# Kernel tuning notes

Measured on AMD Instinct MI355X. Metric: run time of the kernel, lower is better.

The kernel has to match this reference:

```python
import jax, jax.numpy as jnp
import numpy as np

EOS = 1e-10
ALPHA = 0.5
TEMPERATURE = 1.0
BIAS = 0.0001
N_NODES = 8192
N_EDGES = 262144
INPUT_DIM = 512
HIDDEN = 128


def setup_inputs() -> dict:
    key = jax.random.key(0)
    ks = jax.random.split(key, 7)
    features = jax.random.normal(ks[0], (N_NODES, INPUT_DIM), dtype=jnp.float32)
    W_emb = jax.random.normal(ks[1], (HIDDEN, INPUT_DIM), dtype=jnp.float32) * (1.0 / np.sqrt(INPUT_DIM))
    b_emb = jax.random.normal(ks[2], (HIDDEN,), dtype=jnp.float32) * 0.01
    W_edge = jax.random.normal(ks[3], (1, 2 * HIDDEN), dtype=jnp.float32) * (1.0 / np.sqrt(2 * HIDDEN))
    b_edge = jax.random.normal(ks[4], (1,), dtype=jnp.float32) * 0.01
    noise = jax.random.uniform(ks[5], (N_EDGES,), dtype=jnp.float32)
    edges = jax.random.randint(ks[6], (2, N_EDGES), 0, N_NODES, dtype=jnp.int64 if jax.config.jax_enable_x64 else jnp.int32)
    return {"features": features, "W_emb": W_emb, "b_emb": b_emb,
            "W_edge": W_edge, "b_edge": b_edge, "noise": noise, "edges": edges}


def _sym_normalize(adj):
    # inv_sqrt_degree[:,None] * adj * inv_sqrt_degree[None,:]
    inv_sqrt_deg = 1.0 / (jnp.sqrt(adj.sum(axis=1)) + EOS)
    return adj * inv_sqrt_deg[:, None] * inv_sqrt_deg[None, :]


def reference(features, W_emb, b_emb, W_edge, b_edge, noise, edges):
    n = N_NODES
    # node embedding: single Linear + ReLU
    h = jax.nn.relu(features @ W_emb.T + b_emb)            # [N, H]
    e0, e1 = edges[0], edges[1]
    h0, h1 = h[e0], h[e1]                                   # [E, H] gathers
    Wa, Wb = W_edge[0, :HIDDEN], W_edge[0, HIDDEN:]
    s1 = h0 @ Wa + h1 @ Wb + b_edge[0]                       # edge_mlp(cat(h0,h1))
    s2 = h1 @ Wa + h0 @ Wb + b_edge[0]                       # edge_mlp(cat(h1,h0))
    raw = 0.5 * (s1 + s2)                                    # [E]
    # gumbel gate: eps = (bias-(1-bias))*rand + (1-bias)
    eps = (BIAS - (1.0 - BIAS)) * noise + (1.0 - BIAS)
    gate = (jnp.log(eps) - jnp.log1p(-eps) + raw) / TEMPERATURE
    weights_lp = jax.nn.sigmoid(gate)                        # [E]
    weights_hp = 1.0 - weights_lp
    eye = jnp.eye(n, dtype=features.dtype)
    # scatter edge weights to dense adjacency (assignment semantics, like torch adj[e0,e1]=w)
    adj_lp = jnp.zeros((n, n), dtype=features.dtype).at[e0, e1].set(weights_lp) + eye
    adj_lp = _sym_normalize(adj_lp)
    adj_hp = jnp.zeros((n, n), dtype=features.dtype).at[e0, e1].set(weights_hp) + eye
    adj_hp = _sym_normalize(adj_hp)
    mask = jnp.zeros((n, n), dtype=features.dtype).at[e0, e1].set(1.0)
    adj_hp = eye - adj_hp * mask * ALPHA
    return (adj_lp, adj_hp, weights_lp, weights_hp)
```

## Files before the change

### kernel.cpp

```cpp
#include <hip/hip_runtime.h>
#include <cstdint>
#include <cstddef>

#define N_NODES 8192
#define N_EDGES 262144
#define INPUT_DIM 512
#define HIDDEN 128
#define ALPHA 0.5f
#define EOS 1e-10f
#define BCAP 128

typedef float v4 __attribute__((ext_vector_type(4)));
typedef __attribute__((ext_vector_type(8))) short short8;
typedef __attribute__((ext_vector_type(4))) float floatx4;

__device__ inline unsigned short f2bf(float x) {
    unsigned u = __builtin_bit_cast(unsigned, x);
    return (unsigned short)((u + 0x7FFFu + ((u >> 16) & 1u)) >> 16);
}

__global__ __launch_bounds__(256) void k0_conv(
    const float* __restrict__ F, const float* __restrict__ W,
    unsigned short* __restrict__ F16, unsigned short* __restrict__ W16,
    int* __restrict__ cnt)
{
    int t = blockIdx.x * 256 + threadIdx.x;
    if (t < N_NODES) cnt[t] = 0;
    {
        float4 v = *(const float4*)&F[(size_t)t * 4];
        uint2 p;
        p.x = (unsigned)f2bf(v.x) | ((unsigned)f2bf(v.y) << 16);
        p.y = (unsigned)f2bf(v.z) | ((unsigned)f2bf(v.w) << 16);
        *(uint2*)&F16[(size_t)t * 4] = p;
    }
    if (t < 16384) {
        float4 v = *(const float4*)&W[(size_t)t * 4];
        uint2 p;
        p.x = (unsigned)f2bf(v.x) | ((unsigned)f2bf(v.y) << 16);
        p.y = (unsigned)f2bf(v.z) | ((unsigned)f2bf(v.w) << 16);
        *(uint2*)&W16[(size_t)t * 4] = p;
    }
}

__global__ __launch_bounds__(256) void k1_g(
    const unsigned short* __restrict__ F16, const unsigned short* __restrict__ W16,
    const float* __restrict__ bemb, const float* __restrict__ Wedge,
    float* __restrict__ g)
{
    __shared__ float part[4][16];
    int tid = threadIdx.x;
    int lane = tid & 63, wave = tid >> 6;
    int ml = lane & 15, q = lane >> 4;
    int node0 = blockIdx.x * 16;
    int h0 = wave * 32;

    const unsigned short* Ap  = &F16[(size_t)(node0 + ml) * INPUT_DIM + q * 8];
    const unsigned short* Bp0 = &W16[(size_t)(h0 + ml) * INPUT_DIM + q * 8];
    const unsigned short* Bp1 = &W16[(size_t)(h0 + 16 + ml) * INPUT_DIM + q * 8];

    floatx4 acc0 = 0.f, acc1 = 0.f;
#pragma unroll 4
    for (int s = 0; s < 16; s++) {
        short8 a  = *(const short8*)(Ap  + s * 32);
        short8 b0 = *(const short8*)(Bp0 + s * 32);
        short8 b1 = *(const short8*)(Bp1 + s * 32);
        acc0 = __builtin_amdgcn_mfma_f32_16x16x32_bf16(a, b0, acc0, 0, 0, 0);
        acc1 = __builtin_amdgcn_mfma_f32_16x16x32_bf16(a, b1, acc1, 0, 0, 0);
    }
    float sr[4] = {0.f, 0.f, 0.f, 0.f};
#pragma unroll
    for (int t = 0; t < 2; t++) {
        int h = h0 + t * 16 + ml;
        float uu = Wedge[h] + Wedge[HIDDEN + h];
        float bb = bemb[h];
        floatx4 ac = t ? acc1 : acc0;
#pragma unroll
        for (int rg = 0; rg < 4; rg++) {
            float hv = ac[rg] + bb;
            sr[rg] += (hv > 0.f ? hv : 0.f) * uu;
        }
    }
#pragma unroll
    for (int m = 1; m < 16; m <<= 1) {
#pragma unroll
        for (int rg = 0; rg < 4; rg++) sr[rg] += __shfl_xor(sr[rg], m, 64);
    }
    if (ml == 0) {
#pragma unroll
        for (int rg = 0; rg < 4; rg++) part[wave][q * 4 + rg] = sr[rg];
    }
    __syncthreads();
    if (tid < 16)
        g[node0 + tid] = part[0][tid] + part[1][tid] + part[2][tid] + part[3][tid];
}

__global__ __launch_bounds__(256) void k_edge(
    const int* __restrict__ edges, const float* __restrict__ noise,
    const float* __restrict__ g, const float* __restrict__ bedge,
    float* __restrict__ wlp, float* __restrict__ whp,
    int* __restrict__ cnt, int2* __restrict__ buck)
{
    int i = blockIdx.x * 256 + threadIdx.x;
    int e0 = edges[i], e1 = edges[N_EDGES + i];
    float raw = 0.5f * (g[e0] + g[e1]) + bedge[0];
    float eps = -0.9998f * noise[i] + 0.9999f;
    float gate = logf(eps) - log1pf(-eps) + raw;
    float w = 1.f / (1.f + expf(-gate));
    wlp[i] = w;
    whp[i] = 1.f - w;
    int pos = atomicAdd(&cnt[e0], 1);
    if (pos < BCAP) {
        int2 pw;
        pw.x = (e1 << 18) | i;
        pw.y = __builtin_bit_cast(int, w);
        buck[e0 * BCAP + pos] = pw;
    }
}

__global__ __launch_bounds__(256) void k_deginv(
    const int* __restrict__ cnt, int2* __restrict__ buck,
    float* __restrict__ inv_lp, float* __restrict__ inv_hp)
{
    __shared__ int s_pv[2][BCAP];
    __shared__ float plp[4], php[4];
    int tid = threadIdx.x;
    int half = tid >> 7, lt = tid & 127;
    int r = blockIdx.x * 2 + half;
    int d = cnt[r]; if (d > BCAP) d = BCAP;
    int2 pw; pw.x = -1; pw.y = 0;
    if (lt < d) {
        pw = buck[r * BCAP + lt];
        s_pv[half][lt] = pw.x;
    }
    __syncthreads();
    float sl = 0.f, sh = 0.f;
    if (lt < d) {
        int pv = pw.x, c = pv >> 18;
        bool win = true;
        for (int j = 0; j < d; j++) {
            int o = s_pv[half][j];
            if ((o >> 18) == c && o > pv) { win = false; break; }
        }
        if (win) {
            float w = __builtin_bit_cast(float, pw.y);
            sl = w; sh = 1.f - w;
            pw.x = c;
        } else {
            pw.x = -1;
        }
        buck[r * BCAP + lt] = pw;
    }
#pragma unroll
    for (int m = 1; m < 64; m <<= 1) {
        sl += __shfl_xor(sl, m, 64);
        sh += __shfl_xor(sh, m, 64);
    }
    int wv = tid >> 6;
    if ((tid & 63) == 0) { plp[wv] = sl; php[wv] = sh; }
    __syncthreads();
    if (lt == 0) {
        float l = plp[half * 2] + plp[half * 2 + 1];
        float h = php[half * 2] + php[half * 2 + 1];
        inv_lp[r] = 1.f / (sqrtf(l + 1.f) + EOS);
        inv_hp[r] = 1.f / (sqrtf(h + 1.f) + EOS);
    }
}

__global__ __launch_bounds__(256) void k_fill(
    const int* __restrict__ cnt, const int2* __restrict__ buck,
    const float* __restrict__ inv_lp, const float* __restrict__ inv_hp,
    float* __restrict__ LP, float* __restrict__ HP)
{
    __shared__ unsigned bm[256];
    __shared__ unsigned char s_ent[N_NODES];
    __shared__ float s_vlp[BCAP + 1];
    __shared__ float s_vhp[BCAP + 1];
    __shared__ int   s_d;
    int r = blockIdx.x, tid = threadIdx.x;
    bm[tid] = 0;
    int d = cnt[r]; if (d > BCAP) d = BCAP;
    float irl = inv_lp[r], irh = inv_hp[r];
    __syncthreads();
    if (tid < d) {
        int2 pw = buck[r * BCAP + tid];
        int c = pw.x;
        if (c >= 0) {
            float w = __builtin_bit_cast(float, pw.y);
            float icl = inv_lp[c], ich = inv_hp[c];
            float diag = (c == r) ? 1.f : 0.f;
            s_vlp[tid] = (w + diag) * irl * icl;
            s_vhp[tid] = diag - ((1.f - w) + diag) * irh * ich * ALPHA;
            s_ent[c] = (unsigned char)tid;
            atomicOr(&bm[c >> 5], 1u << (c & 31));
        }
    }
    __syncthreads();
    if (tid == 0) {
        if (!((bm[r >> 5] >> (r & 31)) & 1u)) {
            s_vlp[d] = irl * irl; s_vhp[d] = 1.0f;
            s_ent[r] = (unsigned char)d;
            bm[r >> 5] |= 1u << (r & 31);
        }
    }
    __syncthreads();
    float* LPr = LP + (size_t)r * N_NODES;
    float* HPr = HP + (size_t)r * N_NODES;
#pragma unroll
    for (int i = 0; i < 8; i++) {
        int ch = i * 256 + tid;
        unsigned nib = (bm[ch >> 3] >> ((ch & 7) * 4)) & 0xFu;
        v4 lp = 0.f, hp = 0.f;
        if (nib) {
#pragma unroll
            for (int sl = 0; sl < 4; sl++) {
                if (nib & (1u << sl)) {
                    int e = s_ent[ch * 4 + sl];
                    ((float*)&lp)[sl] = s_vlp[e];
                    ((float*)&hp)[sl] = s_vhp[e];
                }
            }
        }
        __builtin_nontemporal_store(lp, (v4*)&LPr[ch * 4]);
        __builtin_nontemporal_store(hp, (v4*)&HPr[ch * 4]);
    }
}

extern "C" void kernel_launch(void* const* d_in, const int* in_sizes, int n_in,
                              void* d_out, int out_size, void* d_ws, size_t ws_size,
                              hipStream_t stream) {
    const float* F     = (const float*)d_in[0];
    const float* W     = (const float*)d_in[1];
    const float* bemb  = (const float*)d_in[2];
    const float* Wedge = (const float*)d_in[3];
    const float* bedge = (const float*)d_in[4];
    const float* noise = (const float*)d_in[5];
    const int*   edges = (const int*)d_in[6];

    const size_t N2 = (size_t)N_NODES * N_NODES;
    float* out = (float*)d_out;
    float* LP  = out;
    float* HP  = out + N2;
    float* wlp = HP + N2;
    float* whp = wlp + N_EDGES;

    char* ws = (char*)d_ws;
    float* g      = (float*)(ws);
    int*   cnt    = (int*)  (ws + 32768);
    float* inv_lp = (float*)(ws + 65536);
    float* inv_hp = (float*)(ws + 98304);
    int2*  buck   = (int2*) (ws + 131072);
    unsigned short* F16 = (unsigned short*)(ws + 131072 + (size_t)N_NODES * BCAP * 8);
    unsigned short* W16 = F16 + (size_t)N_NODES * INPUT_DIM;

    k0_conv<<<4096, 256, 0, stream>>>(F, W, F16, W16, cnt);
    k1_g<<<512, 256, 0, stream>>>(F16, W16, bemb, Wedge, g);
    k_edge<<<N_EDGES / 256, 256, 0, stream>>>(edges, noise, g, bedge,
                                              wlp, whp, cnt, buck);
    k_deginv<<<N_NODES / 2, 256, 0, stream>>>(cnt, buck, inv_lp, inv_hp);
    k_fill<<<N_NODES, 256, 0, stream>>>(cnt, buck, inv_lp, inv_hp, LP, HP);
}
```

Measured before the change: 590.0 us.

## Fuse bf16 conversion into GEMM loads and use regular stores in fill

```diff
diff --git a/kernel.cpp b/kernel.cpp
--- a/kernel.cpp
+++ b/kernel.cpp
@@ -19,51 +19,40 @@
     return (unsigned short)((u + 0x7FFFu + ((u >> 16) & 1u)) >> 16);
 }
 
-__global__ __launch_bounds__(256) void k0_conv(
+__device__ inline short8 ld8bf(const float* __restrict__ p) {
+    float4 u = *(const float4*)p;
+    float4 v = *(const float4*)(p + 4);
+    short8 r;
+    r[0] = (short)f2bf(u.x); r[1] = (short)f2bf(u.y);
+    r[2] = (short)f2bf(u.z); r[3] = (short)f2bf(u.w);
+    r[4] = (short)f2bf(v.x); r[5] = (short)f2bf(v.y);
+    r[6] = (short)f2bf(v.z); r[7] = (short)f2bf(v.w);
+    return r;
+}
+
+__global__ __launch_bounds__(256) void k1_g(
     const float* __restrict__ F, const float* __restrict__ W,
-    unsigned short* __restrict__ F16, unsigned short* __restrict__ W16,
-    int* __restrict__ cnt)
-{
-    int t = blockIdx.x * 256 + threadIdx.x;
-    if (t < N_NODES) cnt[t] = 0;
-    {
-        float4 v = *(const float4*)&F[(size_t)t * 4];
-        uint2 p;
-        p.x = (unsigned)f2bf(v.x) | ((unsigned)f2bf(v.y) << 16);
-        p.y = (unsigned)f2bf(v.z) | ((unsigned)f2bf(v.w) << 16);
-        *(uint2*)&F16[(size_t)t * 4] = p;
-    }
-    if (t < 16384) {
-        float4 v = *(const float4*)&W[(size_t)t * 4];
-        uint2 p;
-        p.x = (unsigned)f2bf(v.x) | ((unsigned)f2bf(v.y) << 16);
-        p.y = (unsigned)f2bf(v.z) | ((unsigned)f2bf(v.w) << 16);
-        *(uint2*)&W16[(size_t)t * 4] = p;
-    }
-}
-
-__global__ __launch_bounds__(256) void k1_g(
-    const unsigned short* __restrict__ F16, const unsigned short* __restrict__ W16,
     const float* __restrict__ bemb, const float* __restrict__ Wedge,
-    float* __restrict__ g)
+    float* __restrict__ g, int* __restrict__ cnt)
 {
     __shared__ float part[4][16];
     int tid = threadIdx.x;
+    int node0 = blockIdx.x * 16;
+    if (tid < 16) cnt[node0 + tid] = 0;
     int lane = tid & 63, wave = tid >> 6;
     int ml = lane & 15, q = lane >> 4;
-    int node0 = blockIdx.x * 16;
     int h0 = wave * 32;
 
-    const unsigned short* Ap  = &F16[(size_t)(node0 + ml) * INPUT_DIM + q * 8];
-    const unsigned short* Bp0 = &W16[(size_t)(h0 + ml) * INPUT_DIM + q * 8];
-    const unsigned short* Bp1 = &W16[(size_t)(h0 + 16 + ml) * INPUT_DIM + q * 8];
+    const float* Ap  = &F[(size_t)(node0 + ml) * INPUT_DIM + q * 8];
+    const float* Bp0 = &W[(size_t)(h0 + ml) * INPUT_DIM + q * 8];
+    const float* Bp1 = &W[(size_t)(h0 + 16 + ml) * INPUT_DIM + q * 8];
 
     floatx4 acc0 = 0.f, acc1 = 0.f;
 #pragma unroll 4
     for (int s = 0; s < 16; s++) {
-        short8 a  = *(const short8*)(Ap  + s * 32);
-        short8 b0 = *(const short8*)(Bp0 + s * 32);
-        short8 b1 = *(const short8*)(Bp1 + s * 32);
+        short8 a  = ld8bf(Ap  + s * 32);
+        short8 b0 = ld8bf(Bp0 + s * 32);
+        short8 b1 = ld8bf(Bp1 + s * 32);
         acc0 = __builtin_amdgcn_mfma_f32_16x16x32_bf16(a, b0, acc0, 0, 0, 0);
         acc1 = __builtin_amdgcn_mfma_f32_16x16x32_bf16(a, b1, acc1, 0, 0, 0);
     }
@@ -175,7 +164,6 @@
     __shared__ unsigned char s_ent[N_NODES];
     __shared__ float s_vlp[BCAP + 1];
     __shared__ float s_vhp[BCAP + 1];
-    __shared__ int   s_d;
     int r = blockIdx.x, tid = threadIdx.x;
     bm[tid] = 0;
     int d = cnt[r]; if (d > BCAP) d = BCAP;
@@ -220,8 +208,8 @@
                 }
             }
         }
-        __builtin_nontemporal_store(lp, (v4*)&LPr[ch * 4]);
-        __builtin_nontemporal_store(hp, (v4*)&HPr[ch * 4]);
+        *(v4*)&LPr[ch * 4] = lp;
+        *(v4*)&HPr[ch * 4] = hp;
     }
 }
 
@@ -249,11 +237,8 @@
     float* inv_lp = (float*)(ws + 65536);
     float* inv_hp = (float*)(ws + 98304);
     int2*  buck   = (int2*) (ws + 131072);
-    unsigned short* F16 = (unsigned short*)(ws + 131072 + (size_t)N_NODES * BCAP * 8);
-    unsigned short* W16 = F16 + (size_t)N_NODES * INPUT_DIM;
-
-    k0_conv<<<4096, 256, 0, stream>>>(F, W, F16, W16, cnt);
-    k1_g<<<512, 256, 0, stream>>>(F16, W16, bemb, Wedge, g);
+
+    k1_g<<<512, 256, 0, stream>>>(F, W, bemb, Wedge, g, cnt);
     k_edge<<<N_EDGES / 256, 256, 0, stream>>>(edges, noise, g, bedge,
                                               wlp, whp, cnt, buck);
     k_deginv<<<N_NODES / 2, 256, 0, stream>>>(cnt, buck, inv_lp, inv_hp);
```

After: 592.6 us. Within noise of the previous version (+0.4%).
